# Optimization experiments

Hardware: AMD Instinct MI355X
Metric: run time of the kernel (lower is better)

## Reference

```python
import jax, jax.numpy as jnp
import numpy as np
import math

D_MODEL = 1024
NUM_HEADS = 16
HEAD_DIM = D_MODEL // NUM_HEADS
B, L = 4, 1024


def setup_inputs() -> dict:
    key = jax.random.key(0)
    ks = jax.random.split(key, 14)
    s = 1.0 / math.sqrt(D_MODEL)
    return {
        "q": jax.random.normal(ks[0], (B, L, D_MODEL), jnp.float32),
        "k": jax.random.normal(ks[1], (B, L, D_MODEL), jnp.float32),
        "v": jax.random.normal(ks[2], (B, L, D_MODEL), jnp.float32),
        "Wq": jax.random.normal(ks[3], (D_MODEL, D_MODEL), jnp.float32) * s,
        "bq": jnp.zeros((D_MODEL,), jnp.float32),
        "Wk": jax.random.normal(ks[4], (D_MODEL, D_MODEL), jnp.float32) * s,
        "bk": jnp.zeros((D_MODEL,), jnp.float32),
        "Wv": jax.random.normal(ks[5], (D_MODEL, D_MODEL), jnp.float32) * s,
        "bv": jnp.zeros((D_MODEL,), jnp.float32),
        "Wo": jax.random.normal(ks[6], (D_MODEL, D_MODEL), jnp.float32) * s,
        "bo": jnp.zeros((D_MODEL,), jnp.float32),
        "lambda_q": jax.random.normal(ks[7], (HEAD_DIM,), jnp.float32) * 0.1,
        "lambda_k": jax.random.normal(ks[8], (HEAD_DIM,), jnp.float32) * 0.1,
        "lambda_v": jax.random.normal(ks[9], (HEAD_DIM,), jnp.float32) * 0.1,
    }


def reference(q, k, v, Wq, bq, Wk, bk, Wv, bv, Wo, bo, lambda_q, lambda_k, lambda_v):
    Bq, Lq, _ = q.shape
    # projections (torch Linear: x @ W.T + b)
    def split_heads(x):
        return x.reshape(Bq, -1, NUM_HEADS, HEAD_DIM).transpose(0, 2, 1, 3)  # [B,H,L,hd]
    qh = split_heads(q @ Wq.T + bq)
    kh = split_heads(k @ Wk.T + bk)
    vh = split_heads(v @ Wv.T + bv)

    lam_self = jnp.exp(jnp.sum(lambda_q * lambda_k))
    lam_cross = jnp.exp(jnp.sum(lambda_k * lambda_v))
    scale = 1.0 / math.sqrt(HEAD_DIM)

    scores_self = jnp.einsum('bhld,bhmd->bhlm', kh, vh) * scale   # [B,H,Lk,Lk]
    scores_cross = jnp.einsum('bhld,bhmd->bhlm', qh, kh) * scale  # [B,H,Lq,Lk]
    scores = scores_cross * lam_cross + scores_self * lam_self

    attn_weights = jax.nn.softmax(jnp.nan_to_num(scores, nan=0.0), axis=-1)
    attn_out = jnp.einsum('bhlm,bhmd->bhld', attn_weights, vh)
    attn_out = attn_out.transpose(0, 2, 1, 3).reshape(Bq, Lq, D_MODEL)
    out = attn_out @ Wo.T + bo
    return (out, attn_weights)
```

## Files before the change

### kernel.cpp

```cpp
#include <hip/hip_runtime.h>
#include <math.h>

#define D_MODEL 1024
#define NHEADS  16
#define HD      64
#define BSZ     4
#define LSEQ    1024
#define BH      64

typedef _Float16 f16;
typedef _Float16 f16x8 __attribute__((ext_vector_type(8)));
typedef _Float16 f16x4 __attribute__((ext_vector_type(4)));
typedef float    f32x4 __attribute__((ext_vector_type(4)));

typedef const __attribute__((address_space(1))) void* gp1_t;
typedef __attribute__((address_space(3))) void* lp3_t;

__device__ __forceinline__ void gload_lds16(const void* g, void* l) {
    __builtin_amdgcn_global_load_lds((gp1_t)g, (lp3_t)l, 16, 0, 0);
}

__global__ void lam_kernel(const float* __restrict__ lq, const float* __restrict__ lk,
                           const float* __restrict__ lv, float* __restrict__ lam) {
    int t = threadIdx.x;
    float pc = lk[t] * lv[t];
    float ps = lq[t] * lk[t];
#pragma unroll
    for (int o = 32; o > 0; o >>= 1) {
        pc += __shfl_down(pc, o, 64);
        ps += __shfl_down(ps, o, 64);
    }
    if (t == 0) {
        float lamC = expf(pc), lamS = expf(ps);
        lam[0] = lamC; lam[1] = lamS;
        lam[2] = lamC / lamS;
        lam[3] = 0.125f * lamS;
    }
}

__global__ __launch_bounds__(256) void cvt4_kernel(
    const float* __restrict__ s0, const float* __restrict__ s1,
    const float* __restrict__ s2, const float* __restrict__ s3,
    f16* __restrict__ d0, f16* __restrict__ d1, f16* __restrict__ d2, f16* __restrict__ d3) {
    int which = blockIdx.y;
    const float* src = which == 0 ? s0 : which == 1 ? s1 : which == 2 ? s2 : s3;
    f16* dst = which == 0 ? d0 : which == 1 ? d1 : which == 2 ? d2 : d3;
    int i = blockIdx.x * blockDim.x + threadIdx.x;
    float4 a = *(const float4*)(src + (size_t)i * 8);
    float4 b = *(const float4*)(src + (size_t)i * 8 + 4);
    f16x8 h;
    h[0]=(f16)a.x; h[1]=(f16)a.y; h[2]=(f16)a.z; h[3]=(f16)a.w;
    h[4]=(f16)b.x; h[5]=(f16)b.y; h[6]=(f16)b.z; h[7]=(f16)b.w;
    *(f16x8*)(dst + (size_t)i * 8) = h;
}

__global__ __launch_bounds__(256, 2) void gemm_qkv_kernel(
    const float* __restrict__ q, const float* __restrict__ k, const float* __restrict__ v,
    const f16* __restrict__ Wq, const f16* __restrict__ Wk, const f16* __restrict__ Wv,
    const float* __restrict__ bq, const float* __restrict__ bk, const float* __restrict__ bv,
    const float* __restrict__ lam,
    f16* __restrict__ Qs, f16* __restrict__ Kh, f16* __restrict__ Vh, f16* __restrict__ Vt)
{
    __shared__ f16 At[2][128 * 64];
    __shared__ f16 Bt[2][128 * 64];

    const int z = blockIdx.z;
    const float* X    = (z == 0) ? q  : (z == 1) ? k  : v;
    const f16*   W    = (z == 0) ? Wq : (z == 1) ? Wk : Wv;
    const float* bias = (z == 0) ? bq : (z == 1) ? bk : bv;

    const int t = threadIdx.x;
    const int lane = t & 63, w = t >> 6;
    const int g = lane >> 4, ln = lane & 15;
    const int wr = w >> 1, wc = w & 1;
    const int n0 = blockIdx.x * 128, m0 = blockIdx.y * 128;
    const int ar = t >> 1, ak = (t & 1) * 32;

    f32x4 acc[4][4];
#pragma unroll
    for (int mi = 0; mi < 4; ++mi)
#pragma unroll
        for (int ni = 0; ni < 4; ++ni)
            acc[mi][ni] = (f32x4){0.f, 0.f, 0.f, 0.f};

    {
        const float* src = X + (size_t)(m0 + ar) * 1024 + ak;
#pragma unroll
        for (int c = 0; c < 4; ++c) {
            float4 f0 = ((const float4*)src)[c * 2];
            float4 f1 = ((const float4*)src)[c * 2 + 1];
            f16x8 hv;
            hv[0]=(f16)f0.x; hv[1]=(f16)f0.y; hv[2]=(f16)f0.z; hv[3]=(f16)f0.w;
            hv[4]=(f16)f1.x; hv[5]=(f16)f1.y; hv[6]=(f16)f1.z; hv[7]=(f16)f1.w;
            int kb = (ak + c * 8) * 2;
            *(f16x8*)((char*)At[0] + ar * 128 + (kb ^ ((ar & 7) << 4))) = hv;
        }
#pragma unroll
        for (int i = 0; i < 4; ++i) {
            int o = t * 16 + i * 4096;
            int r = o >> 7, kb = (o & 127) ^ ((r & 7) << 4);
            gload_lds16(W + (size_t)(n0 + r) * 1024 + (kb >> 1), (char*)Bt[0] + o);
        }
    }
    __syncthreads();

    int cur = 0;
    for (int kt = 0; kt < 16; ++kt) {
        float4 pre[8];
        if (kt < 15) {
            const float* src = X + (size_t)(m0 + ar) * 1024 + (kt + 1) * 64 + ak;
#pragma unroll
            for (int c = 0; c < 8; ++c) pre[c] = ((const float4*)src)[c];
#pragma unroll
            for (int i = 0; i < 4; ++i) {
                int o = t * 16 + i * 4096;
                int r = o >> 7, kb = (o & 127) ^ ((r & 7) << 4);
                gload_lds16(W + (size_t)(n0 + r) * 1024 + (kt + 1) * 64 + (kb >> 1),
                            (char*)Bt[cur ^ 1] + o);
            }
        }
#pragma unroll
        for (int ks = 0; ks < 2; ++ks) {
            f16x8 af[4], bf[4];
#pragma unroll
            for (int mi = 0; mi < 4; ++mi) {
                int r = wr * 64 + mi * 16 + ln;
                af[mi] = *(const f16x8*)((const char*)At[cur] + r * 128 + ((ks * 64 + g * 16) ^ ((r & 7) << 4)));
            }
#pragma unroll
            for (int ni = 0; ni < 4; ++ni) {
                int r = wc * 64 + ni * 16 + ln;
                bf[ni] = *(const f16x8*)((const char*)Bt[cur] + r * 128 + ((ks * 64 + g * 16) ^ ((r & 7) << 4)));
            }
#pragma unroll
            for (int mi = 0; mi < 4; ++mi)
#pragma unroll
                for (int ni = 0; ni < 4; ++ni)
                    acc[mi][ni] = __builtin_amdgcn_mfma_f32_16x16x32_f16(af[mi], bf[ni], acc[mi][ni], 0, 0, 0);
        }
        if (kt < 15) {
#pragma unroll
            for (int c = 0; c < 4; ++c) {
                float4 f0 = pre[c * 2], f1 = pre[c * 2 + 1];
                f16x8 hv;
                hv[0]=(f16)f0.x; hv[1]=(f16)f0.y; hv[2]=(f16)f0.z; hv[3]=(f16)f0.w;
                hv[4]=(f16)f1.x; hv[5]=(f16)f1.y; hv[6]=(f16)f1.z; hv[7]=(f16)f1.w;
                int kb = (ak + c * 8) * 2;
                *(f16x8*)((char*)At[cur ^ 1] + ar * 128 + (kb ^ ((ar & 7) << 4))) = hv;
            }
        }
        __syncthreads();
        cur ^= 1;
    }

    const float alpha = (z == 0) ? lam[2] : 1.0f;
    f16* Y = (z == 0) ? Qs : (z == 1) ? Kh : Vh;
#pragma unroll
    for (int mi = 0; mi < 4; ++mi) {
#pragma unroll
        for (int ni = 0; ni < 4; ++ni) {
            int n = n0 + wc * 64 + ni * 16 + ln;
            int h = n >> 6, d = n & 63;
            float bn = bias[n];
            int mrow0 = m0 + wr * 64 + mi * 16 + 4 * g;
            int b = mrow0 >> 10, l0 = mrow0 & 1023;
            f16x4 tv;
#pragma unroll
            for (int qq = 0; qq < 4; ++qq) {
                float val = (acc[mi][ni][qq] + bn) * alpha;
                f16 hq = (f16)val;
                tv[qq] = hq;
                Y[(((size_t)(b * NHEADS + h)) * LSEQ + l0 + qq) * HD + d] = hq;
            }
            if (z == 2)
                *(f16x4*)(Vt + ((size_t)(b * NHEADS + h) * HD + d) * LSEQ + l0) = tv;
        }
    }
}

__global__ __launch_bounds__(256, 2) void gemm_ao_kernel(
    const f16* __restrict__ A16, const f16* __restrict__ W16,
    const float* __restrict__ bias, float* __restrict__ out)
{
    __shared__ f16 At[2][128 * 64];
    __shared__ f16 Bt[2][128 * 64];

    const int t = threadIdx.x;
    const int lane = t & 63, w = t >> 6;
    const int g = lane >> 4, ln = lane & 15;
    const int wr = w >> 1, wc = w & 1;
    const int n0 = blockIdx.x * 128, m0 = blockIdx.y * 128;

    f32x4 acc[4][4];
#pragma unroll
    for (int mi = 0; mi < 4; ++mi)
#pragma unroll
        for (int ni = 0; ni < 4; ++ni)
            acc[mi][ni] = (f32x4){0.f, 0.f, 0.f, 0.f};

#pragma unroll
    for (int i = 0; i < 4; ++i) {
        int o = t * 16 + i * 4096;
        int r = o >> 7, kb = (o & 127) ^ ((r & 7) << 4);
        gload_lds16(A16 + (size_t)(m0 + r) * 1024 + (kb >> 1), (char*)At[0] + o);
        gload_lds16(W16 + (size_t)(n0 + r) * 1024 + (kb >> 1), (char*)Bt[0] + o);
    }
    __syncthreads();

    int cur = 0;
    for (int kt = 0; kt < 16; ++kt) {
        if (kt < 15) {
#pragma unroll
            for (int i = 0; i < 4; ++i) {
                int o = t * 16 + i * 4096;
                int r = o >> 7, kb = (o & 127) ^ ((r & 7) << 4);
                gload_lds16(A16 + (size_t)(m0 + r) * 1024 + (kt + 1) * 64 + (kb >> 1), (char*)At[cur ^ 1] + o);
                gload_lds16(W16 + (size_t)(n0 + r) * 1024 + (kt + 1) * 64 + (kb >> 1), (char*)Bt[cur ^ 1] + o);
            }
        }
#pragma unroll
        for (int ks = 0; ks < 2; ++ks) {
            f16x8 af[4], bf[4];
#pragma unroll
            for (int mi = 0; mi < 4; ++mi) {
                int r = wr * 64 + mi * 16 + ln;
                af[mi] = *(const f16x8*)((const char*)At[cur] + r * 128 + ((ks * 64 + g * 16) ^ ((r & 7) << 4)));
            }
#pragma unroll
            for (int ni = 0; ni < 4; ++ni) {
                int r = wc * 64 + ni * 16 + ln;
                bf[ni] = *(const f16x8*)((const char*)Bt[cur] + r * 128 + ((ks * 64 + g * 16) ^ ((r & 7) << 4)));
            }
#pragma unroll
            for (int mi = 0; mi < 4; ++mi)
#pragma unroll
                for (int ni = 0; ni < 4; ++ni)
                    acc[mi][ni] = __builtin_amdgcn_mfma_f32_16x16x32_f16(af[mi], bf[ni], acc[mi][ni], 0, 0, 0);
        }
        __syncthreads();
        cur ^= 1;
    }

#pragma unroll
    for (int mi = 0; mi < 4; ++mi)
#pragma unroll
        for (int ni = 0; ni < 4; ++ni) {
            int n = n0 + wc * 64 + ni * 16 + ln;
            float bn = bias[n];
#pragma unroll
            for (int qq = 0; qq < 4; ++qq) {
                int m = m0 + wr * 64 + mi * 16 + 4 * g + qq;
                out[(size_t)m * 1024 + n] = acc[mi][ni][qq] + bn;
            }
        }
}

__global__ __launch_bounds__(512, 4) void attn_kernel(
    const f16* __restrict__ Qs, const f16* __restrict__ Kh, const f16* __restrict__ Vh,
    const f16* __restrict__ Vt, const float* __restrict__ lam,
    float* __restrict__ attnW, f16* __restrict__ AO)
{
    __shared__ char smem[81920];
    char* QtWs = smem;
    char* BtB  = smem + 32768;
    char* VtsB = smem + 65536;

    const int t = threadIdx.x;
    const int lane = t & 63, w = t >> 6;
    const int g = lane >> 4, ln = lane & 15;

    const int bid = blockIdx.x;
    const int wg = (bid & 7) * 64 + (bid >> 3);
    const int bh = wg >> 3, rb = wg & 7;
    const size_t hbase = (size_t)bh * LSEQ * HD;
    const float gamma = lam[3];

    {
        const int r0 = rb * 128;
#pragma unroll
        for (int i = 0; i < 4; ++i) {
            int o = t * 16 + i * 8192;
            int r = o >> 8, kb = (o & 255) ^ ((r & 7) << 4);
            const f16* src = (kb < 128) ? (Qs + hbase + (size_t)(r0 + r) * HD + (kb >> 1))
                                        : (Kh + hbase + (size_t)(r0 + r) * HD + ((kb - 128) >> 1));
            gload_lds16(src, QtWs + o);
        }
    }
#pragma unroll
    for (int i = 0; i < 2; ++i) {
        int o = t * 16 + i * 8192;
        int r = o >> 8, kb = (o & 255) ^ ((r & 7) << 4);
        const f16* src = (kb < 128) ? (Kh + hbase + (size_t)r * HD + (kb >> 1))
                                    : (Vh + hbase + (size_t)r * HD + ((kb - 128) >> 1));
        gload_lds16(src, BtB + o);
    }
    __syncthreads();

    f16x8 qf[4];
    {
        int r = w * 16 + ln;
#pragma unroll
        for (int ks = 0; ks < 4; ++ks)
            qf[ks] = *(const f16x8*)(QtWs + r * 256 + ((ks * 64 + g * 16) ^ ((r & 7) << 4)));
    }

    float lsum = 0.f;
    int cur = 0;
    for (int tt = 0; tt < 16; ++tt) {
        {
            const int c0 = ((tt + 1) & 15) * 64;
#pragma unroll
            for (int i = 0; i < 2; ++i) {
                int o = t * 16 + i * 8192;
                int r = o >> 8, kb = (o & 255) ^ ((r & 7) << 4);
                const f16* src = (kb < 128) ? (Kh + hbase + (size_t)(c0 + r) * HD + (kb >> 1))
                                            : (Vh + hbase + (size_t)(c0 + r) * HD + ((kb - 128) >> 1));
                gload_lds16(src, BtB + (cur ^ 1) * 16384 + o);
            }
            if (tt == 15) {
                int o = t * 16;
                int d = o >> 7, kb = (o & 127) ^ ((d & 7) << 4);
                gload_lds16(Vt + (size_t)bh * HD * LSEQ + (size_t)d * LSEQ + (kb >> 1),
                            VtsB + (cur ^ 1) * 8192 + o);
            }
        }
#pragma unroll
        for (int ci = 0; ci < 4; ++ci) {
            f32x4 acc = (f32x4){0.f, 0.f, 0.f, 0.f};
#pragma unroll
            for (int ks = 0; ks < 4; ++ks) {
                int c = ci * 16 + ln;
                f16x8 af = *(const f16x8*)(BtB + cur * 16384 + c * 256 + ((ks * 64 + g * 16) ^ ((c & 7) << 4)));
                acc = __builtin_amdgcn_mfma_f32_16x16x32_f16(af, qf[ks], acc, 0, 0, 0);
            }
#pragma unroll
            for (int qq = 0; qq < 4; ++qq) lsum += __expf(acc[qq] * gamma);
        }
        __syncthreads();
        cur ^= 1;
    }
    lsum += __shfl_xor(lsum, 16, 64);
    lsum += __shfl_xor(lsum, 32, 64);
    const float il = 1.0f / lsum;

    f32x4 oacc[4];
#pragma unroll
    for (int dj = 0; dj < 4; ++dj) oacc[dj] = (f32x4){0.f, 0.f, 0.f, 0.f};

    for (int tt = 0; tt < 16; ++tt) {
        if (tt < 15) {
            const int c0 = (tt + 1) * 64;
#pragma unroll
            for (int i = 0; i < 2; ++i) {
                int o = t * 16 + i * 8192;
                int r = o >> 8, kb = (o & 255) ^ ((r & 7) << 4);
                const f16* src = (kb < 128) ? (Kh + hbase + (size_t)(c0 + r) * HD + (kb >> 1))
                                            : (Vh + hbase + (size_t)(c0 + r) * HD + ((kb - 128) >> 1));
                gload_lds16(src, BtB + (cur ^ 1) * 16384 + o);
            }
            {
                int o = t * 16;
                int d = o >> 7, kb = (o & 127) ^ ((d & 7) << 4);
                gload_lds16(Vt + (size_t)bh * HD * LSEQ + (size_t)d * LSEQ + c0 + (kb >> 1),
                            VtsB + (cur ^ 1) * 8192 + o);
            }
        }
        {
            const int r = w * 16 + ln;
#pragma unroll
            for (int ci = 0; ci < 4; ++ci) {
                f32x4 acc = (f32x4){0.f, 0.f, 0.f, 0.f};
#pragma unroll
                for (int ks = 0; ks < 4; ++ks) {
                    int c = ci * 16 + ln;
                    f16x8 af = *(const f16x8*)(BtB + cur * 16384 + c * 256 + ((ks * 64 + g * 16) ^ ((c & 7) << 4)));
                    acc = __builtin_amdgcn_mfma_f32_16x16x32_f16(af, qf[ks], acc, 0, 0, 0);
                }
                f32x4 wv;
                wv[0] = __expf(acc[0] * gamma) * il;
                wv[1] = __expf(acc[1] * gamma) * il;
                wv[2] = __expf(acc[2] * gamma) * il;
                wv[3] = __expf(acc[3] * gamma) * il;
                size_t gi = ((size_t)bh * LSEQ + rb * 128 + r) * LSEQ + tt * 64 + ci * 16 + 4 * g;
                __builtin_nontemporal_store(wv, (f32x4*)(attnW + gi));
                f16x4 wh;
                wh[0] = (f16)wv[0]; wh[1] = (f16)wv[1]; wh[2] = (f16)wv[2]; wh[3] = (f16)wv[3];
                *(f16x4*)(QtWs + r * 144 + ci * 32 + g * 8) = wh;
            }
        }
#pragma unroll
        for (int ks = 0; ks < 2; ++ks) {
            int r = w * 16 + ln;
            f16x8 pa = *(const f16x8*)(QtWs + r * 144 + ks * 64 + g * 16);
#pragma unroll
            for (int dj = 0; dj < 4; ++dj) {
                int d = dj * 16 + ln;
                f16x8 vb = *(const f16x8*)(VtsB + cur * 8192 + d * 128 + ((ks * 64 + g * 16) ^ ((d & 7) << 4)));
                oacc[dj] = __builtin_amdgcn_mfma_f32_16x16x32_f16(pa, vb, oacc[dj], 0, 0, 0);
            }
        }
        __syncthreads();
        cur ^= 1;
    }

    {
        const int b = bh >> 4, h = bh & 15;
#pragma unroll
        for (int dj = 0; dj < 4; ++dj)
#pragma unroll
            for (int qq = 0; qq < 4; ++qq) {
                int l = rb * 128 + w * 16 + 4 * g + qq;
                AO[((size_t)b * LSEQ + l) * D_MODEL + h * 64 + dj * 16 + ln] = (f16)oacc[dj][qq];
            }
    }
}

extern "C" void kernel_launch(void* const* d_in, const int* in_sizes, int n_in,
                              void* d_out, int out_size, void* d_ws, size_t ws_size,
                              hipStream_t stream) {
    const float* q  = (const float*)d_in[0];
    const float* k  = (const float*)d_in[1];
    const float* v  = (const float*)d_in[2];
    const float* Wq = (const float*)d_in[3];
    const float* bq = (const float*)d_in[4];
    const float* Wk = (const float*)d_in[5];
    const float* bk = (const float*)d_in[6];
    const float* Wv = (const float*)d_in[7];
    const float* bv = (const float*)d_in[8];
    const float* Wo = (const float*)d_in[9];
    const float* bo = (const float*)d_in[10];
    const float* lq = (const float*)d_in[11];
    const float* lk = (const float*)d_in[12];
    const float* lv = (const float*)d_in[13];

    float* out   = (float*)d_out;
    float* attnW = out + (size_t)BSZ * LSEQ * D_MODEL;

    f16* ws16 = (f16*)d_ws;
    const size_t HSZ = (size_t)BH * LSEQ * HD;
    f16* Qs   = ws16;
    f16* Kh   = ws16 + HSZ;
    f16* Vh   = ws16 + 2 * HSZ;
    f16* Vt   = ws16 + 3 * HSZ;
    f16* AO   = ws16 + 4 * HSZ;
    f16* W16q = ws16 + 5 * HSZ;
    f16* W16k = W16q + 1048576;
    f16* W16v = W16k + 1048576;
    f16* W16o = W16v + 1048576;
    float* lam = (float*)(W16o + 1048576);

    lam_kernel<<<1, 64, 0, stream>>>(lq, lk, lv, lam);

    cvt4_kernel<<<dim3(512, 4), 256, 0, stream>>>(Wq, Wk, Wv, Wo, W16q, W16k, W16v, W16o);

    gemm_qkv_kernel<<<dim3(8, 32, 3), 256, 0, stream>>>(
        q, k, v, W16q, W16k, W16v, bq, bk, bv, lam, Qs, Kh, Vh, Vt);

    attn_kernel<<<512, 512, 0, stream>>>(Qs, Kh, Vh, Vt, lam, attnW, AO);

    gemm_ao_kernel<<<dim3(8, 32), 256, 0, stream>>>(AO, W16o, bo, out);
}
```

Before: 247.7 us.

## Restructure attention into 32-row blocks holding scores in registers; fold lambda into convert

```diff
diff --git a/kernel.cpp b/kernel.cpp
--- a/kernel.cpp
+++ b/kernel.cpp
@@ -20,38 +20,40 @@
     __builtin_amdgcn_global_load_lds((gp1_t)g, (lp3_t)l, 16, 0, 0);
 }
 
-__global__ void lam_kernel(const float* __restrict__ lq, const float* __restrict__ lk,
-                           const float* __restrict__ lv, float* __restrict__ lam) {
-    int t = threadIdx.x;
-    float pc = lk[t] * lv[t];
-    float ps = lq[t] * lk[t];
-#pragma unroll
-    for (int o = 32; o > 0; o >>= 1) {
-        pc += __shfl_down(pc, o, 64);
-        ps += __shfl_down(ps, o, 64);
-    }
-    if (t == 0) {
-        float lamC = expf(pc), lamS = expf(ps);
-        lam[0] = lamC; lam[1] = lamS;
-        lam[2] = lamC / lamS;
-        lam[3] = 0.125f * lamS;
-    }
-}
-
 __global__ __launch_bounds__(256) void cvt4_kernel(
     const float* __restrict__ s0, const float* __restrict__ s1,
     const float* __restrict__ s2, const float* __restrict__ s3,
-    f16* __restrict__ d0, f16* __restrict__ d1, f16* __restrict__ d2, f16* __restrict__ d3) {
+    f16* __restrict__ d0, f16* __restrict__ d1, f16* __restrict__ d2, f16* __restrict__ d3,
+    const float* __restrict__ lq, const float* __restrict__ lk,
+    const float* __restrict__ lv, float* __restrict__ lam) {
     int which = blockIdx.y;
     const float* src = which == 0 ? s0 : which == 1 ? s1 : which == 2 ? s2 : s3;
     f16* dst = which == 0 ? d0 : which == 1 ? d1 : which == 2 ? d2 : d3;
     int i = blockIdx.x * blockDim.x + threadIdx.x;
-    float4 a = *(const float4*)(src + (size_t)i * 8);
-    float4 b = *(const float4*)(src + (size_t)i * 8 + 4);
-    f16x8 h;
-    h[0]=(f16)a.x; h[1]=(f16)a.y; h[2]=(f16)a.z; h[3]=(f16)a.w;
-    h[4]=(f16)b.x; h[5]=(f16)b.y; h[6]=(f16)b.z; h[7]=(f16)b.w;
-    *(f16x8*)(dst + (size_t)i * 8) = h;
+    if (i < 131072) {
+        float4 a = *(const float4*)(src + (size_t)i * 8);
+        float4 b = *(const float4*)(src + (size_t)i * 8 + 4);
+        f16x8 h;
+        h[0]=(f16)a.x; h[1]=(f16)a.y; h[2]=(f16)a.z; h[3]=(f16)a.w;
+        h[4]=(f16)b.x; h[5]=(f16)b.y; h[6]=(f16)b.z; h[7]=(f16)b.w;
+        *(f16x8*)(dst + (size_t)i * 8) = h;
+    }
+    if (blockIdx.x == 0 && blockIdx.y == 0 && threadIdx.x < 64) {
+        int t = threadIdx.x;
+        float pc = lk[t] * lv[t];
+        float ps = lq[t] * lk[t];
+#pragma unroll
+        for (int o = 32; o > 0; o >>= 1) {
+            pc += __shfl_down(pc, o, 64);
+            ps += __shfl_down(ps, o, 64);
+        }
+        if (t == 0) {
+            float lamC = expf(pc), lamS = expf(ps);
+            lam[0] = lamC; lam[1] = lamS;
+            lam[2] = lamC / lamS;
+            lam[3] = 0.125f * lamS;
+        }
+    }
 }
 
 __global__ __launch_bounds__(256, 2) void gemm_qkv_kernel(
@@ -260,158 +262,112 @@
     const f16* __restrict__ Vt, const float* __restrict__ lam,
     float* __restrict__ attnW, f16* __restrict__ AO)
 {
-    __shared__ char smem[81920];
-    char* QtWs = smem;
-    char* BtB  = smem + 32768;
-    char* VtsB = smem + 65536;
+    __shared__ __align__(16) f16 Ws[2][2048];
+    __shared__ float rsum[4][2][16];
 
     const int t = threadIdx.x;
     const int lane = t & 63, w = t >> 6;
     const int g = lane >> 4, ln = lane & 15;
+    const int ci = w & 3, ri = w >> 2;
 
     const int bid = blockIdx.x;
-    const int wg = (bid & 7) * 64 + (bid >> 3);
-    const int bh = wg >> 3, rb = wg & 7;
+    const int wg = (bid & 7) * 256 + (bid >> 3);
+    const int bh = wg >> 5, rb = wg & 31;
     const size_t hbase = (size_t)bh * LSEQ * HD;
     const float gamma = lam[3];
 
-    {
-        const int r0 = rb * 128;
-#pragma unroll
-        for (int i = 0; i < 4; ++i) {
-            int o = t * 16 + i * 8192;
-            int r = o >> 8, kb = (o & 255) ^ ((r & 7) << 4);
-            const f16* src = (kb < 128) ? (Qs + hbase + (size_t)(r0 + r) * HD + (kb >> 1))
-                                        : (Kh + hbase + (size_t)(r0 + r) * HD + ((kb - 128) >> 1));
-            gload_lds16(src, QtWs + o);
-        }
-    }
-#pragma unroll
-    for (int i = 0; i < 2; ++i) {
-        int o = t * 16 + i * 8192;
-        int r = o >> 8, kb = (o & 255) ^ ((r & 7) << 4);
-        const f16* src = (kb < 128) ? (Kh + hbase + (size_t)r * HD + (kb >> 1))
-                                    : (Vh + hbase + (size_t)r * HD + ((kb - 128) >> 1));
-        gload_lds16(src, BtB + o);
-    }
-    __syncthreads();
+    if (t < 128) ((float*)rsum)[t] = 0.f;
 
     f16x8 qf[4];
     {
-        int r = w * 16 + ln;
-#pragma unroll
-        for (int ks = 0; ks < 4; ++ks)
-            qf[ks] = *(const f16x8*)(QtWs + r * 256 + ((ks * 64 + g * 16) ^ ((r & 7) << 4)));
-    }
+        const int qrow = rb * 32 + ri * 16 + ln;
+        const f16* qp = Qs + hbase + (size_t)qrow * HD;
+        const f16* kp = Kh + hbase + (size_t)qrow * HD;
+        qf[0] = *(const f16x8*)(qp + g * 8);
+        qf[1] = *(const f16x8*)(qp + 32 + g * 8);
+        qf[2] = *(const f16x8*)(kp + g * 8);
+        qf[3] = *(const f16x8*)(kp + 32 + g * 8);
+    }
+    __syncthreads();
 
     float lsum = 0.f;
-    int cur = 0;
+    f32x4 sreg[16];
+#pragma unroll
     for (int tt = 0; tt < 16; ++tt) {
-        {
-            const int c0 = ((tt + 1) & 15) * 64;
-#pragma unroll
-            for (int i = 0; i < 2; ++i) {
-                int o = t * 16 + i * 8192;
-                int r = o >> 8, kb = (o & 255) ^ ((r & 7) << 4);
-                const f16* src = (kb < 128) ? (Kh + hbase + (size_t)(c0 + r) * HD + (kb >> 1))
-                                            : (Vh + hbase + (size_t)(c0 + r) * HD + ((kb - 128) >> 1));
-                gload_lds16(src, BtB + (cur ^ 1) * 16384 + o);
-            }
-            if (tt == 15) {
-                int o = t * 16;
-                int d = o >> 7, kb = (o & 127) ^ ((d & 7) << 4);
-                gload_lds16(Vt + (size_t)bh * HD * LSEQ + (size_t)d * LSEQ + (kb >> 1),
-                            VtsB + (cur ^ 1) * 8192 + o);
-            }
-        }
-#pragma unroll
-        for (int ci = 0; ci < 4; ++ci) {
-            f32x4 acc = (f32x4){0.f, 0.f, 0.f, 0.f};
-#pragma unroll
-            for (int ks = 0; ks < 4; ++ks) {
-                int c = ci * 16 + ln;
-                f16x8 af = *(const f16x8*)(BtB + cur * 16384 + c * 256 + ((ks * 64 + g * 16) ^ ((c & 7) << 4)));
-                acc = __builtin_amdgcn_mfma_f32_16x16x32_f16(af, qf[ks], acc, 0, 0, 0);
-            }
-#pragma unroll
-            for (int qq = 0; qq < 4; ++qq) lsum += __expf(acc[qq] * gamma);
-        }
-        __syncthreads();
-        cur ^= 1;
+        const f16* kr = Kh + hbase + (size_t)(tt * 64 + ci * 16 + ln) * HD;
+        const f16* vr = Vh + hbase + (size_t)(tt * 64 + ci * 16 + ln) * HD;
+        f16x8 a0 = *(const f16x8*)(kr + g * 8);
+        f16x8 a1 = *(const f16x8*)(kr + 32 + g * 8);
+        f16x8 a2 = *(const f16x8*)(vr + g * 8);
+        f16x8 a3 = *(const f16x8*)(vr + 32 + g * 8);
+        f32x4 acc = (f32x4){0.f, 0.f, 0.f, 0.f};
+        acc = __builtin_amdgcn_mfma_f32_16x16x32_f16(a0, qf[0], acc, 0, 0, 0);
+        acc = __builtin_amdgcn_mfma_f32_16x16x32_f16(a1, qf[1], acc, 0, 0, 0);
+        acc = __builtin_amdgcn_mfma_f32_16x16x32_f16(a2, qf[2], acc, 0, 0, 0);
+        acc = __builtin_amdgcn_mfma_f32_16x16x32_f16(a3, qf[3], acc, 0, 0, 0);
+        f32x4 e;
+        e[0] = __expf(acc[0] * gamma);
+        e[1] = __expf(acc[1] * gamma);
+        e[2] = __expf(acc[2] * gamma);
+        e[3] = __expf(acc[3] * gamma);
+        lsum += (e[0] + e[1]) + (e[2] + e[3]);
+        sreg[tt] = e;
     }
     lsum += __shfl_xor(lsum, 16, 64);
     lsum += __shfl_xor(lsum, 32, 64);
-    const float il = 1.0f / lsum;
-
-    f32x4 oacc[4];
-#pragma unroll
-    for (int dj = 0; dj < 4; ++dj) oacc[dj] = (f32x4){0.f, 0.f, 0.f, 0.f};
-
+    if (g == 0) rsum[ci][ri][ln] = lsum;
+    __syncthreads();
+    const float il = 1.0f / ((rsum[0][ri][ln] + rsum[1][ri][ln]) +
+                             (rsum[2][ri][ln] + rsum[3][ri][ln]));
+
+    const int dj = w & 3, rb2 = w >> 2;
+    const int r1 = ri * 16 + ln;
+    const int r2 = rb2 * 16 + ln;
+    const int dd = dj * 16 + ln;
+    const f16* vtrow = Vt + (size_t)bh * HD * LSEQ + (size_t)dd * LSEQ;
+    f32x4 oacc = (f32x4){0.f, 0.f, 0.f, 0.f};
+
+    f16x8 vb0 = *(const f16x8*)(vtrow + g * 8);
+    f16x8 vb1 = *(const f16x8*)(vtrow + 32 + g * 8);
+
+    const int wsw = (32 * ci + 8 * g) ^ ((r1 & 7) << 4);
+    const int psw0 = (16 * g) ^ ((r2 & 7) << 4);
+    const int psw1 = (64 + 16 * g) ^ ((r2 & 7) << 4);
+
+#pragma unroll
     for (int tt = 0; tt < 16; ++tt) {
+        const int p = tt & 1;
+        f32x4 wv = sreg[tt] * il;
+        {
+            f16x4 wh;
+            wh[0] = (f16)wv[0]; wh[1] = (f16)wv[1];
+            wh[2] = (f16)wv[2]; wh[3] = (f16)wv[3];
+            *(f16x4*)((char*)Ws[p] + r1 * 128 + wsw) = wh;
+        }
+        {
+            size_t gi = ((size_t)bh * LSEQ + rb * 32 + r1) * LSEQ + tt * 64 + ci * 16 + 4 * g;
+            __builtin_nontemporal_store(wv, (f32x4*)(attnW + gi));
+        }
+        __syncthreads();
+        f16x8 nvb0, nvb1;
         if (tt < 15) {
-            const int c0 = (tt + 1) * 64;
-#pragma unroll
-            for (int i = 0; i < 2; ++i) {
-                int o = t * 16 + i * 8192;
-                int r = o >> 8, kb = (o & 255) ^ ((r & 7) << 4);
-                const f16* src = (kb < 128) ? (Kh + hbase + (size_t)(c0 + r) * HD + (kb >> 1))
-                                            : (Vh + hbase + (size_t)(c0 + r) * HD + ((kb - 128) >> 1));
-                gload_lds16(src, BtB + (cur ^ 1) * 16384 + o);
-            }
-            {
-                int o = t * 16;
-                int d = o >> 7, kb = (o & 127) ^ ((d & 7) << 4);
-                gload_lds16(Vt + (size_t)bh * HD * LSEQ + (size_t)d * LSEQ + c0 + (kb >> 1),
-                            VtsB + (cur ^ 1) * 8192 + o);
-            }
-        }
-        {
-            const int r = w * 16 + ln;
-#pragma unroll
-            for (int ci = 0; ci < 4; ++ci) {
-                f32x4 acc = (f32x4){0.f, 0.f, 0.f, 0.f};
-#pragma unroll
-                for (int ks = 0; ks < 4; ++ks) {
-                    int c = ci * 16 + ln;
-                    f16x8 af = *(const f16x8*)(BtB + cur * 16384 + c * 256 + ((ks * 64 + g * 16) ^ ((c & 7) << 4)));
-                    acc = __builtin_amdgcn_mfma_f32_16x16x32_f16(af, qf[ks], acc, 0, 0, 0);
-                }
-                f32x4 wv;
-                wv[0] = __expf(acc[0] * gamma) * il;
-                wv[1] = __expf(acc[1] * gamma) * il;
-                wv[2] = __expf(acc[2] * gamma) * il;
-                wv[3] = __expf(acc[3] * gamma) * il;
-                size_t gi = ((size_t)bh * LSEQ + rb * 128 + r) * LSEQ + tt * 64 + ci * 16 + 4 * g;
-                __builtin_nontemporal_store(wv, (f32x4*)(attnW + gi));
-                f16x4 wh;
-                wh[0] = (f16)wv[0]; wh[1] = (f16)wv[1]; wh[2] = (f16)wv[2]; wh[3] = (f16)wv[3];
-                *(f16x4*)(QtWs + r * 144 + ci * 32 + g * 8) = wh;
-            }
-        }
-#pragma unroll
-        for (int ks = 0; ks < 2; ++ks) {
-            int r = w * 16 + ln;
-            f16x8 pa = *(const f16x8*)(QtWs + r * 144 + ks * 64 + g * 16);
-#pragma unroll
-            for (int dj = 0; dj < 4; ++dj) {
-                int d = dj * 16 + ln;
-                f16x8 vb = *(const f16x8*)(VtsB + cur * 8192 + d * 128 + ((ks * 64 + g * 16) ^ ((d & 7) << 4)));
-                oacc[dj] = __builtin_amdgcn_mfma_f32_16x16x32_f16(pa, vb, oacc[dj], 0, 0, 0);
-            }
-        }
-        __syncthreads();
-        cur ^= 1;
+            nvb0 = *(const f16x8*)(vtrow + (tt + 1) * 64 + g * 8);
+            nvb1 = *(const f16x8*)(vtrow + (tt + 1) * 64 + 32 + g * 8);
+        }
+        f16x8 pa0 = *(const f16x8*)((const char*)Ws[p] + r2 * 128 + psw0);
+        f16x8 pa1 = *(const f16x8*)((const char*)Ws[p] + r2 * 128 + psw1);
+        oacc = __builtin_amdgcn_mfma_f32_16x16x32_f16(pa0, vb0, oacc, 0, 0, 0);
+        oacc = __builtin_amdgcn_mfma_f32_16x16x32_f16(pa1, vb1, oacc, 0, 0, 0);
+        vb0 = nvb0; vb1 = nvb1;
     }
 
     {
         const int b = bh >> 4, h = bh & 15;
 #pragma unroll
-        for (int dj = 0; dj < 4; ++dj)
-#pragma unroll
-            for (int qq = 0; qq < 4; ++qq) {
-                int l = rb * 128 + w * 16 + 4 * g + qq;
-                AO[((size_t)b * LSEQ + l) * D_MODEL + h * 64 + dj * 16 + ln] = (f16)oacc[dj][qq];
-            }
+        for (int qq = 0; qq < 4; ++qq) {
+            int l = rb * 32 + rb2 * 16 + 4 * g + qq;
+            AO[((size_t)b * LSEQ + l) * D_MODEL + h * 64 + dd] = (f16)oacc[qq];
+        }
     }
 }
 
@@ -449,14 +405,13 @@
     f16* W16o = W16v + 1048576;
     float* lam = (float*)(W16o + 1048576);
 
-    lam_kernel<<<1, 64, 0, stream>>>(lq, lk, lv, lam);
-
-    cvt4_kernel<<<dim3(512, 4), 256, 0, stream>>>(Wq, Wk, Wv, Wo, W16q, W16k, W16v, W16o);
+    cvt4_kernel<<<dim3(512, 4), 256, 0, stream>>>(Wq, Wk, Wv, Wo, W16q, W16k, W16v, W16o,
+                                                  lq, lk, lv, lam);
 
     gemm_qkv_kernel<<<dim3(8, 32, 3), 256, 0, stream>>>(
         q, k, v, W16q, W16k, W16v, bq, bk, bv, lam, Qs, Kh, Vh, Vt);
 
-    attn_kernel<<<512, 512, 0, stream>>>(Qs, Kh, Vh, Vt, lam, attnW, AO);
+    attn_kernel<<<2048, 512, 0, stream>>>(Qs, Kh, Vh, Vt, lam, attnW, AO);
 
     gemm_ao_kernel<<<dim3(8, 32), 256, 0, stream>>>(AO, W16o, bo, out);
 }
```

Result: slower. 309.2 us (+24.8%).
